# Kernel optimization log

Measured on AMD Instinct MI355X. Metric: run time of the kernel, lower is better.

The kernel has to match this reference:

```python
import jax, jax.numpy as jnp
import numpy as np

B, N, D = 8, 8192, 3
C = 64
M = 2048          # num_samples
K = 32            # max_neighbors
RADIUS = 0.3
OUT = 128
EXP = 4
CIN = C + D       # 67
HID = CIN * EXP   # 268
EPS = 1e-6        # flax LayerNorm default


def setup_inputs() -> dict:
    key = jax.random.key(0)
    ks = jax.random.split(key, 6)
    return {
        "x": jax.random.normal(ks[0], (B, N, D), jnp.float32),
        "features": jax.random.normal(ks[1], (B, N, C), jnp.float32),
        "first_idx": jax.random.randint(ks[2], (B,), 0, N, jnp.int32),
        "w1": jax.random.normal(ks[3], (CIN, HID), jnp.float32) / np.float32(np.sqrt(CIN)),
        "b1": jnp.zeros((HID,), jnp.float32),
        "g1": jnp.ones((HID,), jnp.float32),
        "be1": jnp.zeros((HID,), jnp.float32),
        "w2": jax.random.normal(ks[4], (HID, OUT), jnp.float32) / np.float32(np.sqrt(HID)),
        "b2": jnp.zeros((OUT,), jnp.float32),
        "g2": jnp.ones((OUT,), jnp.float32),
        "be2": jnp.zeros((OUT,), jnp.float32),
    }


def _layernorm(h, g, b):
    mu = jnp.mean(h, axis=-1, keepdims=True)
    var = jnp.mean(jnp.square(h), axis=-1, keepdims=True) - jnp.square(mu)
    return (h - mu) * jax.lax.rsqrt(var + EPS) * g + b


def _fps(x, first_idx, num_samples):
    # Sequential farthest-point sampling via lax.scan.
    batch = jnp.arange(x.shape[0])
    sel = jnp.full((x.shape[0], num_samples), -1, dtype=jnp.int32)
    sel = sel.at[:, 0].set(first_idx)
    first_pts = x[batch, first_idx]                       # (B,3)
    dists = jnp.sum((x - first_pts[:, None, :]) ** 2, -1)  # (B,N)

    def step(carry, i):
        s, d = carry
        far = jnp.argmax(d, axis=-1)
        s = s.at[:, i].set(far.astype(jnp.int32))
        fp = x[batch, far]
        d = jnp.minimum(d, jnp.sum((x - fp[:, None, :]) ** 2, -1))
        return (s, d), None

    (sel, _), _ = jax.lax.scan(step, (sel, dists), jnp.arange(1, num_samples))
    return sel


def _ball_query(centers, points, radius, max_neighbors):
    # centers (B,M,3), points (B,N,3) -> (B,M,K) indices, -1 where invalid
    d2 = jnp.sum((centers[:, :, None, :] - points[:, None, :, :]) ** 2, -1)  # (B,M,N)
    within = d2 < radius ** 2
    nbr = jnp.argsort(jnp.where(within, d2, 1e10), axis=-1)[:, :, :max_neighbors]
    nd = jnp.take_along_axis(d2, nbr, axis=-1)
    return jnp.where(nd < radius ** 2, nbr, -1)


def reference(x, features, first_idx, w1, b1, g1, be1, w2, b2, g2, be2):
    batch = jnp.arange(B)[:, None]                 # (B,1)
    sel = _fps(x, first_idx, M)                    # (B,M)
    centers = x[batch, sel]                        # (B,M,3)
    nbr = _ball_query(centers, x, RADIUS, K)       # (B,M,K); -1 wraps to last point (as original)
    bI = batch[:, :, None]                         # (B,1,1)
    nf = features[bI, nbr]                         # (B,M,K,C)
    npts = x[bI, nbr]                              # (B,M,K,3)
    rel = npts - centers[:, :, None, :]
    comb = jnp.concatenate([nf, rel], axis=-1)     # (B,M,K,C+3)
    h = jax.nn.gelu(comb @ w1 + b1)                # (B,M,K,HID), tanh-approx gelu as flax default
    h = _layernorm(h, g1, be1)
    h = h @ w2 + b2                                # (B,M,K,OUT)
    h = _layernorm(h, g2, be2)
    out = jnp.max(h, axis=2)                       # (B,M,OUT)
    return (centers, out)
```

## Files before the change

kernel.cpp:

```cpp
#include <hip/hip_runtime.h>
#include <hip/hip_bf16.h>
#include <math.h>

#define B_ 8
#define N_ 8192
#define C_ 64
#define M_ 2048
#define K_ 32
#define OUT_ 128
#define CIN_ 67
#define HID_ 268
#define EPS_ 1e-6f
#define CONS_ 240
#define CAPQ_ 512

typedef short short8 __attribute__((ext_vector_type(8)));
typedef float floatx4 __attribute__((ext_vector_type(4)));

__device__ __forceinline__ unsigned short f2bf(float f) {
  unsigned u = __builtin_bit_cast(unsigned, f);
  u += 0x7fffu + ((u >> 16) & 1u);
  return (unsigned short)(u >> 16);
}
__device__ __forceinline__ float bf2f(unsigned short h) {
  return __builtin_bit_cast(float, (unsigned)h << 16);
}

__device__ __forceinline__ float d2fma(float ax, float ay, float az,
                                       float bx, float by, float bz) {
#pragma clang fp contract(off)
  float dx = ax - bx, dy = ay - by, dz = az - bz;
  return __builtin_fmaf(dz, dz, __builtin_fmaf(dy, dy, dx * dx));
}

__device__ __forceinline__ float gelu_tanh(float v) {
  const float k0 = 0.7978845608028654f;
  const float k1 = 0.044715f;
  float u = k0 * (v + k1 * v * v * v);
  return 0.5f * v * (1.0f + tanhf(u));
}

__device__ __forceinline__ int msp4(int v) {
  return (v & 1) | ((v & 2) << 2) | ((v & 4) << 4) | ((v & 8) << 6);
}

template <int CTRL>
__device__ __forceinline__ unsigned long long dpp_umax64(unsigned long long k) {
  int lo = (int)(unsigned)k;
  int hi = (int)(unsigned)(k >> 32);
  unsigned slo = (unsigned)__builtin_amdgcn_update_dpp(0, lo, CTRL, 0xF, 0xF, true);
  unsigned shi = (unsigned)__builtin_amdgcn_update_dpp(0, hi, CTRL, 0xF, 0xF, true);
  unsigned long long o = ((unsigned long long)shi << 32) | (unsigned long long)slo;
  return k > o ? k : o;
}

__global__ __launch_bounds__(256) void pack_kernel(
    const float* __restrict__ w1, const float* __restrict__ w2,
    unsigned short* __restrict__ w1p, unsigned short* __restrict__ w2p,
    int* __restrict__ prog) {
  if (blockIdx.x == 0) prog[threadIdx.x] = 0;
  int e = blockIdx.x * 256 + threadIdx.x;
  if (e < 3 * 17 * 64 * 8) {
    int j = e & 7, lane = (e >> 3) & 63, fi = e >> 9;
    int kt = fi / 17, nt = fi - kt * 17;
    int k = kt * 32 + (lane >> 4) * 8 + j;
    int n = nt * 16 + (lane & 15);
    float v = (k < CIN_ && n < HID_) ? w1[k * HID_ + n] : 0.f;
    w1p[e] = f2bf(v);
  } else {
    int e2 = e - 3 * 17 * 64 * 8;
    if (e2 < 9 * 8 * 64 * 8) {
      int j = e2 & 7, lane = (e2 >> 3) & 63, fi = e2 >> 9;
      int kt = fi >> 3, nt = fi & 7;
      int k = kt * 32 + (lane >> 4) * 8 + j;
      int n = nt * 16 + (lane & 15);
      float v = (k < HID_) ? w2[k * OUT_ + n] : 0.f;
      w2p[e2] = f2bf(v);
    }
  }
}

__global__ __launch_bounds__(512) void fused_kernel(
    const float* __restrict__ x, const float* __restrict__ features,
    const int* __restrict__ first_idx,
    const unsigned short* __restrict__ w1p, const float* __restrict__ b1,
    const float* __restrict__ g1, const float* __restrict__ be1,
    const unsigned short* __restrict__ w2p, const float* __restrict__ b2,
    const float* __restrict__ g2, const float* __restrict__ be2,
    float* __restrict__ centers, float* __restrict__ out1,
    int* __restrict__ prog) {
  __shared__ __align__(16) char smem[131456];
  const int tid = threadIdx.x;
  const int lane = tid & 63;
  const int wv = tid >> 6;

  if (blockIdx.x < B_) {
    const int b = blockIdx.x;
    const float* xb = x + (size_t)b * N_ * 3;

    float* s_xyz = (float*)smem;
    char* s_mem = smem + 98304;
    unsigned long long* s_wkey = (unsigned long long*)(smem + 131072);
    int* s_wsum = (int*)(smem + 131200);
    float* s_bb = (float*)(smem + 131232);

    int* s_hist = (int*)s_mem;
    unsigned short* s_perm = (unsigned short*)(s_mem + 16384);
    float* s_cbuf = (float*)s_mem;

    {
      const float4* src = (const float4*)xb;
      float4* dst = (float4*)s_xyz;
#pragma unroll
      for (int i = 0; i < 12; ++i) {
        int e = tid + i * 512;
        dst[e] = src[e];
      }
    }
    for (int i = tid; i < 4096; i += 512) s_hist[i] = 0;
    __syncthreads();

    float bx0 = INFINITY, bx1 = -INFINITY, by0 = INFINITY, by1 = -INFINITY,
          bz0 = INFINITY, bz1 = -INFINITY;
#pragma unroll
    for (int i = 0; i < 16; ++i) {
      int p = tid + i * 512;
      float X = s_xyz[p * 3 + 0], Y = s_xyz[p * 3 + 1], Z = s_xyz[p * 3 + 2];
      bx0 = fminf(bx0, X); bx1 = fmaxf(bx1, X);
      by0 = fminf(by0, Y); by1 = fmaxf(by1, Y);
      bz0 = fminf(bz0, Z); bz1 = fmaxf(bz1, Z);
    }
#pragma unroll
    for (int off = 1; off < 64; off <<= 1) {
      bx0 = fminf(bx0, __shfl_xor(bx0, off)); bx1 = fmaxf(bx1, __shfl_xor(bx1, off));
      by0 = fminf(by0, __shfl_xor(by0, off)); by1 = fmaxf(by1, __shfl_xor(by1, off));
      bz0 = fminf(bz0, __shfl_xor(bz0, off)); bz1 = fmaxf(bz1, __shfl_xor(bz1, off));
    }
    if (lane == 0) {
      s_bb[wv * 6 + 0] = bx0; s_bb[wv * 6 + 1] = bx1; s_bb[wv * 6 + 2] = by0;
      s_bb[wv * 6 + 3] = by1; s_bb[wv * 6 + 4] = bz0; s_bb[wv * 6 + 5] = bz1;
    }
    __syncthreads();
#pragma unroll
    for (int w = 0; w < 8; ++w) {
      bx0 = fminf(bx0, s_bb[w * 6 + 0]); bx1 = fmaxf(bx1, s_bb[w * 6 + 1]);
      by0 = fminf(by0, s_bb[w * 6 + 2]); by1 = fmaxf(by1, s_bb[w * 6 + 3]);
      bz0 = fminf(bz0, s_bb[w * 6 + 4]); bz1 = fmaxf(bz1, s_bb[w * 6 + 5]);
    }
    const float kS = 16.0f * (1.0f - 1e-6f);
    float rx = bx1 - bx0, ry = by1 - by0, rz = bz1 - bz0;
    float sxv = rx > 0.f ? kS / rx : 0.f;
    float syv = ry > 0.f ? kS / ry : 0.f;
    float szv = rz > 0.f ? kS / rz : 0.f;

#pragma unroll
    for (int i = 0; i < 16; ++i) {
      int p = tid + i * 512;
      int qx = (int)((s_xyz[p * 3 + 0] - bx0) * sxv);
      int qy = (int)((s_xyz[p * 3 + 1] - by0) * syv);
      int qz = (int)((s_xyz[p * 3 + 2] - bz0) * szv);
      qx = qx < 0 ? 0 : (qx > 15 ? 15 : qx);
      qy = qy < 0 ? 0 : (qy > 15 ? 15 : qy);
      qz = qz < 0 ? 0 : (qz > 15 ? 15 : qz);
      int c = msp4(qx) | (msp4(qy) << 1) | (msp4(qz) << 2);
      atomicAdd(&s_hist[c], 1);
    }
    __syncthreads();

    {
      int h[8], pre[8];
      int acc = 0;
#pragma unroll
      for (int i = 0; i < 8; ++i) { h[i] = s_hist[tid * 8 + i]; pre[i] = acc; acc += h[i]; }
      int incl = acc;
#pragma unroll
      for (int off = 1; off < 64; off <<= 1) {
        int v = __shfl_up(incl, off);
        if (lane >= off) incl += v;
      }
      int texcl = incl - acc;
      if (lane == 63) s_wsum[wv] = incl;
      __syncthreads();
      int woff = 0;
#pragma unroll
      for (int w = 0; w < 8; ++w) woff += (w < wv) ? s_wsum[w] : 0;
#pragma unroll
      for (int i = 0; i < 8; ++i) s_hist[tid * 8 + i] = woff + texcl + pre[i];
    }
    __syncthreads();

#pragma unroll
    for (int i = 0; i < 16; ++i) {
      int p = tid + i * 512;
      int qx = (int)((s_xyz[p * 3 + 0] - bx0) * sxv);
      int qy = (int)((s_xyz[p * 3 + 1] - by0) * syv);
      int qz = (int)((s_xyz[p * 3 + 2] - bz0) * szv);
      qx = qx < 0 ? 0 : (qx > 15 ? 15 : qx);
      qy = qy < 0 ? 0 : (qy > 15 ? 15 : qy);
      qz = qz < 0 ? 0 : (qz > 15 ? 15 : qz);
      int c = msp4(qx) | (msp4(qy) << 1) | (msp4(qz) << 2);
      int pos = atomicAdd(&s_hist[c], 1);
      s_perm[pos] = (unsigned short)p;
    }
    __syncthreads();

    float px[16], py[16], pz[16], d[16];
    unsigned lo32[16];
    float gx0[2], gx1[2], gy0[2], gy1[2], gz0[2], gz1[2];
#pragma unroll
    for (int g = 0; g < 2; ++g) {
      gx0[g] = INFINITY; gx1[g] = -INFINITY; gy0[g] = INFINITY;
      gy1[g] = -INFINITY; gz0[g] = INFINITY; gz1[g] = -INFINITY;
    }
#pragma unroll
    for (int i = 0; i < 16; ++i) {
      int p = (int)s_perm[tid * 16 + i];
      int g = i >> 3;
      px[i] = s_xyz[p * 3 + 0];
      py[i] = s_xyz[p * 3 + 1];
      pz[i] = s_xyz[p * 3 + 2];
      d[i] = INFINITY;
      lo32[i] = 0xFFFFFFFFu - (unsigned)p;
      gx0[g] = fminf(gx0[g], px[i]); gx1[g] = fmaxf(gx1[g], px[i]);
      gy0[g] = fminf(gy0[g], py[i]); gy1[g] = fmaxf(gy1[g], py[i]);
      gz0[g] = fminf(gz0[g], pz[i]); gz1[g] = fmaxf(gz1[g], pz[i]);
    }
    float wx0 = fminf(gx0[0], gx0[1]), wx1 = fmaxf(gx1[0], gx1[1]);
    float wy0 = fminf(gy0[0], gy0[1]), wy1 = fmaxf(gy1[0], gy1[1]);
    float wz0 = fminf(gz0[0], gz0[1]), wz1 = fmaxf(gz1[0], gz1[1]);
#pragma unroll
    for (int off = 1; off < 64; off <<= 1) {
      wx0 = fminf(wx0, __shfl_xor(wx0, off)); wx1 = fmaxf(wx1, __shfl_xor(wx1, off));
      wy0 = fminf(wy0, __shfl_xor(wy0, off)); wy1 = fmaxf(wy1, __shfl_xor(wy1, off));
      wz0 = fminf(wz0, __shfl_xor(wz0, off)); wz1 = fmaxf(wz1, __shfl_xor(wz1, off));
    }

    int fi = first_idx[b];
    float ncx = s_xyz[fi * 3 + 0], ncy = s_xyz[fi * 3 + 1], ncz = s_xyz[fi * 3 + 2];
    if (tid == 0) {
      s_cbuf[0] = ncx; s_cbuf[1] = ncy; s_cbuf[2] = ncz;
    }

    unsigned long long gkey[2];
    gkey[0] = 0x7F800000ULL << 32;
    gkey[1] = 0x7F800000ULL << 32;
    unsigned long long wk = 0x7F800000ULL << 32;

    for (int it = 1; it < M_; ++it) {
      float wdx = fmaxf(fmaxf(wx0 - ncx, ncx - wx1), 0.f);
      float wdy = fmaxf(fmaxf(wy0 - ncy, ncy - wy1), 0.f);
      float wdz = fmaxf(fmaxf(wz0 - ncz, ncz - wz1), 0.f);
      float wlb = __builtin_fmaf(wdz, wdz, __builtin_fmaf(wdy, wdy, wdx * wdx));
      float wgm = __builtin_bit_cast(float, (unsigned)(wk >> 32));
      if (__any(wlb * 0.999f < wgm)) {
#pragma unroll
        for (int g = 0; g < 2; ++g) {
          float gdx = fmaxf(fmaxf(gx0[g] - ncx, ncx - gx1[g]), 0.f);
          float gdy = fmaxf(fmaxf(gy0[g] - ncy, ncy - gy1[g]), 0.f);
          float gdz = fmaxf(fmaxf(gz0[g] - ncz, ncz - gz1[g]), 0.f);
          float glb = __builtin_fmaf(gdz, gdz, __builtin_fmaf(gdy, gdy, gdx * gdx));
          float ggm = __builtin_bit_cast(float, (unsigned)(gkey[g] >> 32));
          if (glb * 0.999f < ggm) {
            unsigned long long k[8];
#pragma unroll
            for (int i = 0; i < 8; ++i) {
              int s = g * 8 + i;
              float dd = d2fma(px[s], py[s], pz[s], ncx, ncy, ncz);
              float dm = fminf(d[s], dd);
              d[s] = dm;
              k[i] = ((unsigned long long)__builtin_bit_cast(unsigned, dm) << 32) |
                     (unsigned long long)lo32[s];
            }
#pragma unroll
            for (int sd = 4; sd >= 1; sd >>= 1)
#pragma unroll
              for (int i = 0; i < sd; ++i)
                k[i] = k[i] > k[i + sd] ? k[i] : k[i + sd];
            gkey[g] = k[0];
          }
        }
        unsigned long long kk = gkey[0] > gkey[1] ? gkey[0] : gkey[1];
        kk = dpp_umax64<0x111>(kk);
        kk = dpp_umax64<0x112>(kk);
        kk = dpp_umax64<0x114>(kk);
        kk = dpp_umax64<0x118>(kk);
        kk = dpp_umax64<0x142>(kk);
        kk = dpp_umax64<0x143>(kk);
        wk = kk;
      }
      if (lane == 63) s_wkey[(it & 1) * 8 + wv] = wk;
      __syncthreads();
      if ((it & 31) == 0) {
        if (wv == 0 && lane < 24) {
          const float4* src = (const float4*)(s_cbuf + (size_t)(it - 32) * 3);
          float4* dst = (float4*)(centers + (size_t)b * M_ * 3 + (size_t)(it - 32) * 3);
          dst[lane] = src[lane];
        }
        if (tid == 0)
          __hip_atomic_store(&prog[b * 32], it, __ATOMIC_RELEASE, __HIP_MEMORY_SCOPE_AGENT);
      }
      {
        const ulonglong2* sp = (const ulonglong2*)(&s_wkey[(it & 1) * 8]);
        ulonglong2 q0 = sp[0], q1 = sp[1], q2 = sp[2], q3 = sp[3];
        unsigned long long a0 = q0.x > q0.y ? q0.x : q0.y;
        unsigned long long a1 = q1.x > q1.y ? q1.x : q1.y;
        unsigned long long a2 = q2.x > q2.y ? q2.x : q2.y;
        unsigned long long a3 = q3.x > q3.y ? q3.x : q3.y;
        unsigned long long b0 = a0 > a1 ? a0 : a1;
        unsigned long long b1v = a2 > a3 ? a2 : a3;
        unsigned long long gk = b0 > b1v ? b0 : b1v;
        int gi = (int)(0xFFFFFFFFu - (unsigned)(gk & 0xFFFFFFFFull));
        int gs = __builtin_amdgcn_readfirstlane(gi);
        ncx = s_xyz[gs * 3 + 0];
        ncy = s_xyz[gs * 3 + 1];
        ncz = s_xyz[gs * 3 + 2];
      }
      if (tid == 0) {
        s_cbuf[it * 3 + 0] = ncx; s_cbuf[it * 3 + 1] = ncy; s_cbuf[it * 3 + 2] = ncz;
      }
    }

    __syncthreads();
    if (wv == 0 && lane < 24) {
      const float4* src = (const float4*)(s_cbuf + (size_t)(M_ - 32) * 3);
      float4* dst = (float4*)(centers + (size_t)b * M_ * 3 + (size_t)(M_ - 32) * 3);
      dst[lane] = src[lane];
    }
    if (tid == 0)
      __hip_atomic_store(&prog[b * 32], M_, __ATOMIC_RELEASE, __HIP_MEMORY_SCOPE_AGENT);

  } else {
    unsigned short* A1 = (unsigned short*)smem;
    unsigned short* H1 = (unsigned short*)(smem + 13312);
    float* H2 = (float*)(smem + 51200);
    float* cd = (float*)(smem + 84992);
    int* cidx = (int*)(smem + 89088);
    float* s_sum = (float*)(smem + 93184);
    float* s_sum2 = (float*)(smem + 93440);
    float* s_mu = (float*)(smem + 93696);
    float* s_rs = (float*)(smem + 93952);
    int* s_nbr = (int*)(smem + 94208);
    float* s_ctr = (float*)(smem + 94464);
    int* s_wc = (int*)(smem + 94496);

    const int j = (int)blockIdx.x - B_;
    const int b = j & 7;
    const int c = j >> 3;
    const int q4 = lane >> 4;
    const int nl = lane & 15;

    for (int e = tid; e < 64 * 104; e += 512) A1[e] = 0;
    for (int e = tid; e < 64 * 296; e += 512) H1[e] = 0;
    __syncthreads();

    const float* xb = x + (size_t)b * N_ * 3;

    for (int k35 = 0; k35 < 35; ++k35) {
      int i = c + 30 * k35;
      if (i >= 1024) break;
      const int m0 = 2 * i, m1 = m0 + 1;
      const int cm0 = b * M_ + m0;

      if (tid == 0) {
        if (__hip_atomic_load(&prog[b * 32], __ATOMIC_ACQUIRE,
                              __HIP_MEMORY_SCOPE_AGENT) <= m1) {
          do {
            __builtin_amdgcn_s_sleep(16);
          } while (__hip_atomic_load(&prog[b * 32], __ATOMIC_ACQUIRE,
                                     __HIP_MEMORY_SCOPE_AGENT) <= m1);
        }
      }
      __syncthreads();

      if (tid < 64) s_sum[tid] = 0.f;
      else if (tid < 128) s_sum2[tid - 64] = 0.f;
      else if (tid < 134) s_ctr[tid - 128] = centers[(size_t)cm0 * 3 + (tid - 128)];
      __syncthreads();

      const float c0x = s_ctr[0], c0y = s_ctr[1], c0z = s_ctr[2];
      const float c1x = s_ctr[3], c1y = s_ctr[4], c1z = s_ctr[5];

      int cnt0 = 0, cnt1 = 0;
      for (int s = 0; s < 16; ++s) {
        int p = wv * 1024 + s * 64 + lane;
        float X = xb[p * 3 + 0], Y = xb[p * 3 + 1], Z = xb[p * 3 + 2];
        float d20 = d2fma(X, Y, Z, c0x, c0y, c0z);
        float d21 = d2fma(X, Y, Z, c1x, c1y, c1z);
        cnt0 += (int)__popcll(__ballot(d20 < 0.09f));
        cnt1 += (int)__popcll(__ballot(d21 < 0.09f));
      }
      if (lane == 0) { s_wc[wv] = cnt0; s_wc[8 + wv] = cnt1; }
      __syncthreads();
      int base0 = 0, tot0 = 0, base1 = 0, tot1 = 0;
#pragma unroll
      for (int w = 0; w < 8; ++w) {
        int v0 = s_wc[w], v1 = s_wc[8 + w];
        base0 += (w < wv) ? v0 : 0; tot0 += v0;
        base1 += (w < wv) ? v1 : 0; tot1 += v1;
      }
      int count0 = tot0 < CAPQ_ ? tot0 : CAPQ_;
      int count1 = tot1 < CAPQ_ ? tot1 : CAPQ_;
      int pos0 = base0, pos1 = base1;
      for (int s = 0; s < 16; ++s) {
        int p = wv * 1024 + s * 64 + lane;
        float X = xb[p * 3 + 0], Y = xb[p * 3 + 1], Z = xb[p * 3 + 2];
        float d20 = d2fma(X, Y, Z, c0x, c0y, c0z);
        float d21 = d2fma(X, Y, Z, c1x, c1y, c1z);
        bool in0 = d20 < 0.09f;
        bool in1 = d21 < 0.09f;
        unsigned long long m0m = __ballot(in0);
        unsigned long long m1m = __ballot(in1);
        if (in0) {
          int pp = pos0 + (int)__popcll(m0m & ((1ull << lane) - 1ull));
          if (pp < CAPQ_) { cd[pp] = d20; cidx[pp] = p; }
        }
        if (in1) {
          int pp = pos1 + (int)__popcll(m1m & ((1ull << lane) - 1ull));
          if (pp < CAPQ_) { cd[CAPQ_ + pp] = d21; cidx[CAPQ_ + pp] = p; }
        }
        pos0 += (int)__popcll(m0m);
        pos1 += (int)__popcll(m1m);
      }
      __syncthreads();
      {
        int q = tid >> 8;
        int lt = tid & 255;
        int cnt = q ? count1 : count0;
        int nw = cnt < K_ ? cnt : K_;
        const float* cdq = cd + q * CAPQ_;
        const int* cxq = cidx + q * CAPQ_;
        for (int cc = lt; cc < cnt; cc += 256) {
          float dcc = cdq[cc];
          int rank = 0;
          for (int jj = 0; jj < cnt; ++jj) {
            float dj = cdq[jj];
            rank += (dj < dcc || (dj == dcc && jj < cc)) ? 1 : 0;
          }
          if (rank < K_) s_nbr[q * K_ + rank] = cxq[cc];
        }
        for (int s = nw + lt; s < K_; s += 256) s_nbr[q * K_ + s] = N_ - 1;
      }
      __syncthreads();

#pragma unroll
      for (int h = 0; h < 2; ++h) {
        int rr = (tid >> 4) + h * 32;
        int jj = tid & 15;
        int q = rr >> 5;
        int idx = s_nbr[rr];
        const float4* frow = (const float4*)(features + ((size_t)b * N_ + idx) * C_);
        float4 f4 = frow[jj];
        int base = rr * 104 + jj * 4;
        A1[base + 0] = f2bf(f4.x); A1[base + 1] = f2bf(f4.y);
        A1[base + 2] = f2bf(f4.z); A1[base + 3] = f2bf(f4.w);
        if (jj == 0) {
          const float* xp = x + ((size_t)b * N_ + idx) * 3;
          A1[rr * 104 + 64] = f2bf(xp[0] - s_ctr[q * 3 + 0]);
          A1[rr * 104 + 65] = f2bf(xp[1] - s_ctr[q * 3 + 1]);
          A1[rr * 104 + 66] = f2bf(xp[2] - s_ctr[q * 3 + 2]);
        }
      }
      __syncthreads();

      for (int nt = wv; nt < 17; nt += 8) {
        short8 bfr[3];
#pragma unroll
        for (int kt = 0; kt < 3; ++kt)
          bfr[kt] = *(const short8*)(w1p + (size_t)((kt * 17 + nt) * 64 + lane) * 8);
        int col = nt * 16 + nl;
        bool cok = col < HID_;
        float bias = cok ? b1[col] : 0.f;
#pragma unroll
        for (int mt = 0; mt < 4; ++mt) {
          floatx4 acc = {0.f, 0.f, 0.f, 0.f};
          const unsigned short* ap = A1 + (mt * 16 + nl) * 104 + q4 * 8;
#pragma unroll
          for (int kt = 0; kt < 3; ++kt) {
            short8 a = *(const short8*)(ap + kt * 32);
            acc = __builtin_amdgcn_mfma_f32_16x16x32_bf16(a, bfr[kt], acc, 0, 0, 0);
          }
#pragma unroll
          for (int r = 0; r < 4; ++r) {
            int row = mt * 16 + q4 * 4 + r;
            float g = 0.f;
            if (cok) {
              float v = acc[r] + bias;
              g = gelu_tanh(v);
              H1[row * 296 + col] = f2bf(g);
            }
            float s1 = g, s2 = g * g;
#pragma unroll
            for (int off = 1; off < 16; off <<= 1) {
              s1 += __shfl_xor(s1, off);
              s2 += __shfl_xor(s2, off);
            }
            if (nl == 0) { atomicAdd(&s_sum[row], s1); atomicAdd(&s_sum2[row], s2); }
          }
        }
      }
      __syncthreads();
      if (tid < 64) {
        float mu = s_sum[tid] * (1.f / HID_);
        float var = s_sum2[tid] * (1.f / HID_) - mu * mu;
        s_mu[tid] = mu;
        s_rs[tid] = rsqrtf(var + EPS_);
      }
      __syncthreads();
      for (int e = tid; e < 64 * HID_; e += 512) {
        int r = e / HID_, cc = e - r * HID_;
        float g = bf2f(H1[r * 296 + cc]);
        float v = (g - s_mu[r]) * s_rs[r] * g1[cc] + be1[cc];
        H1[r * 296 + cc] = f2bf(v);
      }
      if (tid < 64) { s_sum[tid] = 0.f; s_sum2[tid] = 0.f; }
      __syncthreads();

      {
        int nt = wv;
        short8 bfr2[9];
#pragma unroll
        for (int kt = 0; kt < 9; ++kt)
          bfr2[kt] = *(const short8*)(w2p + (size_t)((kt * 8 + nt) * 64 + lane) * 8);
        int col = nt * 16 + nl;
        float bias = b2[col];
#pragma unroll
        for (int mt = 0; mt < 4; ++mt) {
          floatx4 acc = {0.f, 0.f, 0.f, 0.f};
          const unsigned short* ap = H1 + (mt * 16 + nl) * 296 + q4 * 8;
#pragma unroll
          for (int kt = 0; kt < 9; ++kt) {
            short8 a = *(const short8*)(ap + kt * 32);
            acc = __builtin_amdgcn_mfma_f32_16x16x32_bf16(a, bfr2[kt], acc, 0, 0, 0);
          }
#pragma unroll
          for (int r = 0; r < 4; ++r) {
            int row = mt * 16 + q4 * 4 + r;
            float v = acc[r] + bias;
            H2[row * 132 + col] = v;
            float s1 = v, s2 = v * v;
#pragma unroll
            for (int off = 1; off < 16; off <<= 1) {
              s1 += __shfl_xor(s1, off);
              s2 += __shfl_xor(s2, off);
            }
            if (nl == 0) { atomicAdd(&s_sum[row], s1); atomicAdd(&s_sum2[row], s2); }
          }
        }
      }
      __syncthreads();
      if (tid < 64) {
        float mu = s_sum[tid] * (1.f / OUT_);
        float var = s_sum2[tid] * (1.f / OUT_) - mu * mu;
        s_mu[tid] = mu;
        s_rs[tid] = rsqrtf(var + EPS_);
      }
      __syncthreads();
      if (tid < 256) {
        int q = tid >> 7, col = tid & 127;
        float gg = g2[col], bb = be2[col];
        float mx = -3.4e38f;
#pragma unroll 4
        for (int r = 0; r < K_; ++r) {
          int row = q * K_ + r;
          float v = H2[row * 132 + col];
          float o = (v - s_mu[row]) * s_rs[row] * gg + bb;
          mx = fmaxf(mx, o);
        }
        out1[(size_t)(cm0 + q) * OUT_ + col] = mx;
      }
      __syncthreads();
    }
  }
}

extern "C" void kernel_launch(void* const* d_in, const int* in_sizes, int n_in,
                              void* d_out, int out_size, void* d_ws, size_t ws_size,
                              hipStream_t stream) {
  const float* x = (const float*)d_in[0];
  const float* features = (const float*)d_in[1];
  const int* first_idx = (const int*)d_in[2];
  const float* w1 = (const float*)d_in[3];
  const float* b1 = (const float*)d_in[4];
  const float* g1 = (const float*)d_in[5];
  const float* be1 = (const float*)d_in[6];
  const float* w2 = (const float*)d_in[7];
  const float* b2 = (const float*)d_in[8];
  const float* g2 = (const float*)d_in[9];
  const float* be2 = (const float*)d_in[10];

  float* centers = (float*)d_out;
  float* out1 = (float*)d_out + (size_t)B_ * M_ * 3;

  int* prog = (int*)d_ws;
  unsigned short* w1p = (unsigned short*)((char*)d_ws + 2097152);
  unsigned short* w2p = (unsigned short*)((char*)d_ws + 2149376);

  pack_kernel<<<dim3(246), dim3(256), 0, stream>>>(w1, w2, w1p, w2p, prog);
  fused_kernel<<<dim3(B_ + CONS_), dim3(512), 0, stream>>>(
      x, features, first_idx, w1p, b1, g1, be1, w2p, b2, g2, be2,
      centers, out1, prog);
}
```

Before: 1.943 ms.

## Run two interleaved FPS batches per producer block sharing one barrier

Each producer block now runs farthest-point sampling for two batches at once, each thread holding 32 points in registers, and one __syncthreads per iteration serves both batches. The idea is to let the independent dependency chains of two batches hide each other's latency and to halve the number of producer blocks. Other changes: the per-wave bounding-box early-out is dropped, centers are staged through a small 64-entry ring instead of a full buffer, the next center is read from global memory instead of LDS, and consumer spin-waits use relaxed loads with periodic acquire. Risks are higher register pressure and a longer per-iteration critical path, since each block now does twice the serial work.

```diff
diff --git a/kernel.cpp b/kernel.cpp
--- a/kernel.cpp
+++ b/kernel.cpp
@@ -11,6 +11,7 @@
 #define CIN_ 67
 #define HID_ 268
 #define EPS_ 1e-6f
+#define NPROD_ 4
 #define CONS_ 240
 #define CAPQ_ 512
 
@@ -52,6 +53,16 @@
   unsigned shi = (unsigned)__builtin_amdgcn_update_dpp(0, hi, CTRL, 0xF, 0xF, true);
   unsigned long long o = ((unsigned long long)shi << 32) | (unsigned long long)slo;
   return k > o ? k : o;
+}
+
+__device__ __forceinline__ unsigned long long wave_dpp_max64(unsigned long long kk) {
+  kk = dpp_umax64<0x111>(kk);
+  kk = dpp_umax64<0x112>(kk);
+  kk = dpp_umax64<0x114>(kk);
+  kk = dpp_umax64<0x118>(kk);
+  kk = dpp_umax64<0x142>(kk);
+  kk = dpp_umax64<0x143>(kk);
+  return kk;
 }
 
 __global__ __launch_bounds__(256) void pack_kernel(
@@ -89,218 +100,224 @@
     const float* __restrict__ g2, const float* __restrict__ be2,
     float* __restrict__ centers, float* __restrict__ out1,
     int* __restrict__ prog) {
-  __shared__ __align__(16) char smem[131456];
+  __shared__ __align__(16) char smem[133632];
   const int tid = threadIdx.x;
   const int lane = tid & 63;
   const int wv = tid >> 6;
 
-  if (blockIdx.x < B_) {
-    const int b = blockIdx.x;
-    const float* xb = x + (size_t)b * N_ * 3;
+  if (blockIdx.x < NPROD_) {
+    const int bp = blockIdx.x;
 
     float* s_xyz = (float*)smem;
-    char* s_mem = smem + 98304;
-    unsigned long long* s_wkey = (unsigned long long*)(smem + 131072);
-    int* s_wsum = (int*)(smem + 131200);
-    float* s_bb = (float*)(smem + 131232);
-
-    int* s_hist = (int*)s_mem;
-    unsigned short* s_perm = (unsigned short*)(s_mem + 16384);
-    float* s_cbuf = (float*)s_mem;
-
-    {
-      const float4* src = (const float4*)xb;
-      float4* dst = (float4*)s_xyz;
-#pragma unroll
-      for (int i = 0; i < 12; ++i) {
-        int e = tid + i * 512;
-        dst[e] = src[e];
-      }
+    int* s_hist = (int*)(smem + 98304);
+    unsigned short* s_perm = (unsigned short*)(smem + 114688);
+    float* s_ring0 = (float*)(smem + 131072);
+    float* s_ring1 = (float*)(smem + 131840);
+    unsigned long long* s_went = (unsigned long long*)(smem + 132608);
+    int* s_wsum = (int*)(smem + 132864);
+    float* s_bb = (float*)(smem + 132896);
+
+    float px[32], py[32], pz[32], d[32];
+    unsigned lo32[32];
+    float gx0[2][2], gx1[2][2], gy0[2][2], gy1[2][2], gz0[2][2], gz1[2][2];
+    float ncx[2], ncy[2], ncz[2];
+
+#pragma unroll
+    for (int h = 0; h < 2; ++h) {
+      const int b = 2 * bp + h;
+      const float* xb = x + (size_t)b * N_ * 3;
+
+      {
+        const float4* src = (const float4*)xb;
+        float4* dst = (float4*)s_xyz;
+#pragma unroll
+        for (int i = 0; i < 12; ++i) {
+          int e = tid + i * 512;
+          dst[e] = src[e];
+        }
+      }
+      for (int i = tid; i < 4096; i += 512) s_hist[i] = 0;
+      __syncthreads();
+
+      float bx0 = INFINITY, bx1 = -INFINITY, by0 = INFINITY, by1 = -INFINITY,
+            bz0 = INFINITY, bz1 = -INFINITY;
+#pragma unroll
+      for (int i = 0; i < 16; ++i) {
+        int p = tid + i * 512;
+        float X = s_xyz[p * 3 + 0], Y = s_xyz[p * 3 + 1], Z = s_xyz[p * 3 + 2];
+        bx0 = fminf(bx0, X); bx1 = fmaxf(bx1, X);
+        by0 = fminf(by0, Y); by1 = fmaxf(by1, Y);
+        bz0 = fminf(bz0, Z); bz1 = fmaxf(bz1, Z);
+      }
+#pragma unroll
+      for (int off = 1; off < 64; off <<= 1) {
+        bx0 = fminf(bx0, __shfl_xor(bx0, off)); bx1 = fmaxf(bx1, __shfl_xor(bx1, off));
+        by0 = fminf(by0, __shfl_xor(by0, off)); by1 = fmaxf(by1, __shfl_xor(by1, off));
+        bz0 = fminf(bz0, __shfl_xor(bz0, off)); bz1 = fmaxf(bz1, __shfl_xor(bz1, off));
+      }
+      if (lane == 0) {
+        s_bb[wv * 6 + 0] = bx0; s_bb[wv * 6 + 1] = bx1; s_bb[wv * 6 + 2] = by0;
+        s_bb[wv * 6 + 3] = by1; s_bb[wv * 6 + 4] = bz0; s_bb[wv * 6 + 5] = bz1;
+      }
+      __syncthreads();
+#pragma unroll
+      for (int w = 0; w < 8; ++w) {
+        bx0 = fminf(bx0, s_bb[w * 6 + 0]); bx1 = fmaxf(bx1, s_bb[w * 6 + 1]);
+        by0 = fminf(by0, s_bb[w * 6 + 2]); by1 = fmaxf(by1, s_bb[w * 6 + 3]);
+        bz0 = fminf(bz0, s_bb[w * 6 + 4]); bz1 = fmaxf(bz1, s_bb[w * 6 + 5]);
+      }
+      const float kS = 16.0f * (1.0f - 1e-6f);
+      float rx = bx1 - bx0, ry = by1 - by0, rz = bz1 - bz0;
+      float sxv = rx > 0.f ? kS / rx : 0.f;
+      float syv = ry > 0.f ? kS / ry : 0.f;
+      float szv = rz > 0.f ? kS / rz : 0.f;
+
+#pragma unroll
+      for (int i = 0; i < 16; ++i) {
+        int p = tid + i * 512;
+        int qx = (int)((s_xyz[p * 3 + 0] - bx0) * sxv);
+        int qy = (int)((s_xyz[p * 3 + 1] - by0) * syv);
+        int qz = (int)((s_xyz[p * 3 + 2] - bz0) * szv);
+        qx = qx < 0 ? 0 : (qx > 15 ? 15 : qx);
+        qy = qy < 0 ? 0 : (qy > 15 ? 15 : qy);
+        qz = qz < 0 ? 0 : (qz > 15 ? 15 : qz);
+        int cc = msp4(qx) | (msp4(qy) << 1) | (msp4(qz) << 2);
+        atomicAdd(&s_hist[cc], 1);
+      }
+      __syncthreads();
+
+      {
+        int hh[8], pre[8];
+        int acc = 0;
+#pragma unroll
+        for (int i = 0; i < 8; ++i) { hh[i] = s_hist[tid * 8 + i]; pre[i] = acc; acc += hh[i]; }
+        int incl = acc;
+#pragma unroll
+        for (int off = 1; off < 64; off <<= 1) {
+          int v = __shfl_up(incl, off);
+          if (lane >= off) incl += v;
+        }
+        int texcl = incl - acc;
+        if (lane == 63) s_wsum[wv] = incl;
+        __syncthreads();
+        int woff = 0;
+#pragma unroll
+        for (int w = 0; w < 8; ++w) woff += (w < wv) ? s_wsum[w] : 0;
+#pragma unroll
+        for (int i = 0; i < 8; ++i) s_hist[tid * 8 + i] = woff + texcl + pre[i];
+      }
+      __syncthreads();
+
+#pragma unroll
+      for (int i = 0; i < 16; ++i) {
+        int p = tid + i * 512;
+        int qx = (int)((s_xyz[p * 3 + 0] - bx0) * sxv);
+        int qy = (int)((s_xyz[p * 3 + 1] - by0) * syv);
+        int qz = (int)((s_xyz[p * 3 + 2] - bz0) * szv);
+        qx = qx < 0 ? 0 : (qx > 15 ? 15 : qx);
+        qy = qy < 0 ? 0 : (qy > 15 ? 15 : qy);
+        qz = qz < 0 ? 0 : (qz > 15 ? 15 : qz);
+        int cc = msp4(qx) | (msp4(qy) << 1) | (msp4(qz) << 2);
+        int pos = atomicAdd(&s_hist[cc], 1);
+        s_perm[pos] = (unsigned short)p;
+      }
+      __syncthreads();
+
+#pragma unroll
+      for (int g = 0; g < 2; ++g) {
+        gx0[h][g] = INFINITY; gx1[h][g] = -INFINITY; gy0[h][g] = INFINITY;
+        gy1[h][g] = -INFINITY; gz0[h][g] = INFINITY; gz1[h][g] = -INFINITY;
+      }
+#pragma unroll
+      for (int i = 0; i < 16; ++i) {
+        int p = (int)s_perm[tid * 16 + i];
+        int g = i >> 3;
+        int s = h * 16 + i;
+        px[s] = s_xyz[p * 3 + 0];
+        py[s] = s_xyz[p * 3 + 1];
+        pz[s] = s_xyz[p * 3 + 2];
+        d[s] = INFINITY;
+        lo32[s] = 0xFFFFFFFFu - (unsigned)p;
+        gx0[h][g] = fminf(gx0[h][g], px[s]); gx1[h][g] = fmaxf(gx1[h][g], px[s]);
+        gy0[h][g] = fminf(gy0[h][g], py[s]); gy1[h][g] = fmaxf(gy1[h][g], py[s]);
+        gz0[h][g] = fminf(gz0[h][g], pz[s]); gz1[h][g] = fmaxf(gz1[h][g], pz[s]);
+      }
+
+      int fi = first_idx[b];
+      ncx[h] = s_xyz[fi * 3 + 0]; ncy[h] = s_xyz[fi * 3 + 1]; ncz[h] = s_xyz[fi * 3 + 2];
+      if (tid == 0) {
+        float* r = (h ? s_ring1 : s_ring0);
+        r[0] = ncx[h]; r[1] = ncy[h]; r[2] = ncz[h];
+      }
+      __syncthreads();
     }
-    for (int i = tid; i < 4096; i += 512) s_hist[i] = 0;
-    __syncthreads();
-
-    float bx0 = INFINITY, bx1 = -INFINITY, by0 = INFINITY, by1 = -INFINITY,
-          bz0 = INFINITY, bz1 = -INFINITY;
-#pragma unroll
-    for (int i = 0; i < 16; ++i) {
-      int p = tid + i * 512;
-      float X = s_xyz[p * 3 + 0], Y = s_xyz[p * 3 + 1], Z = s_xyz[p * 3 + 2];
-      bx0 = fminf(bx0, X); bx1 = fmaxf(bx1, X);
-      by0 = fminf(by0, Y); by1 = fmaxf(by1, Y);
-      bz0 = fminf(bz0, Z); bz1 = fmaxf(bz1, Z);
-    }
-#pragma unroll
-    for (int off = 1; off < 64; off <<= 1) {
-      bx0 = fminf(bx0, __shfl_xor(bx0, off)); bx1 = fmaxf(bx1, __shfl_xor(bx1, off));
-      by0 = fminf(by0, __shfl_xor(by0, off)); by1 = fmaxf(by1, __shfl_xor(by1, off));
-      bz0 = fminf(bz0, __shfl_xor(bz0, off)); bz1 = fmaxf(bz1, __shfl_xor(bz1, off));
-    }
-    if (lane == 0) {
-      s_bb[wv * 6 + 0] = bx0; s_bb[wv * 6 + 1] = bx1; s_bb[wv * 6 + 2] = by0;
-      s_bb[wv * 6 + 3] = by1; s_bb[wv * 6 + 4] = bz0; s_bb[wv * 6 + 5] = bz1;
-    }
-    __syncthreads();
-#pragma unroll
-    for (int w = 0; w < 8; ++w) {
-      bx0 = fminf(bx0, s_bb[w * 6 + 0]); bx1 = fmaxf(bx1, s_bb[w * 6 + 1]);
-      by0 = fminf(by0, s_bb[w * 6 + 2]); by1 = fmaxf(by1, s_bb[w * 6 + 3]);
-      bz0 = fminf(bz0, s_bb[w * 6 + 4]); bz1 = fmaxf(bz1, s_bb[w * 6 + 5]);
-    }
-    const float kS = 16.0f * (1.0f - 1e-6f);
-    float rx = bx1 - bx0, ry = by1 - by0, rz = bz1 - bz0;
-    float sxv = rx > 0.f ? kS / rx : 0.f;
-    float syv = ry > 0.f ? kS / ry : 0.f;
-    float szv = rz > 0.f ? kS / rz : 0.f;
-
-#pragma unroll
-    for (int i = 0; i < 16; ++i) {
-      int p = tid + i * 512;
-      int qx = (int)((s_xyz[p * 3 + 0] - bx0) * sxv);
-      int qy = (int)((s_xyz[p * 3 + 1] - by0) * syv);
-      int qz = (int)((s_xyz[p * 3 + 2] - bz0) * szv);
-      qx = qx < 0 ? 0 : (qx > 15 ? 15 : qx);
-      qy = qy < 0 ? 0 : (qy > 15 ? 15 : qy);
-      qz = qz < 0 ? 0 : (qz > 15 ? 15 : qz);
-      int c = msp4(qx) | (msp4(qy) << 1) | (msp4(qz) << 2);
-      atomicAdd(&s_hist[c], 1);
-    }
-    __syncthreads();
-
-    {
-      int h[8], pre[8];
-      int acc = 0;
-#pragma unroll
-      for (int i = 0; i < 8; ++i) { h[i] = s_hist[tid * 8 + i]; pre[i] = acc; acc += h[i]; }
-      int incl = acc;
-#pragma unroll
-      for (int off = 1; off < 64; off <<= 1) {
-        int v = __shfl_up(incl, off);
-        if (lane >= off) incl += v;
-      }
-      int texcl = incl - acc;
-      if (lane == 63) s_wsum[wv] = incl;
-      __syncthreads();
-      int woff = 0;
-#pragma unroll
-      for (int w = 0; w < 8; ++w) woff += (w < wv) ? s_wsum[w] : 0;
-#pragma unroll
-      for (int i = 0; i < 8; ++i) s_hist[tid * 8 + i] = woff + texcl + pre[i];
-    }
-    __syncthreads();
-
-#pragma unroll
-    for (int i = 0; i < 16; ++i) {
-      int p = tid + i * 512;
-      int qx = (int)((s_xyz[p * 3 + 0] - bx0) * sxv);
-      int qy = (int)((s_xyz[p * 3 + 1] - by0) * syv);
-      int qz = (int)((s_xyz[p * 3 + 2] - bz0) * szv);
-      qx = qx < 0 ? 0 : (qx > 15 ? 15 : qx);
-      qy = qy < 0 ? 0 : (qy > 15 ? 15 : qy);
-      qz = qz < 0 ? 0 : (qz > 15 ? 15 : qz);
-      int c = msp4(qx) | (msp4(qy) << 1) | (msp4(qz) << 2);
-      int pos = atomicAdd(&s_hist[c], 1);
-      s_perm[pos] = (unsigned short)p;
-    }
-    __syncthreads();
-
-    float px[16], py[16], pz[16], d[16];
-    unsigned lo32[16];
-    float gx0[2], gx1[2], gy0[2], gy1[2], gz0[2], gz1[2];
-#pragma unroll
-    for (int g = 0; g < 2; ++g) {
-      gx0[g] = INFINITY; gx1[g] = -INFINITY; gy0[g] = INFINITY;
-      gy1[g] = -INFINITY; gz0[g] = INFINITY; gz1[g] = -INFINITY;
-    }
-#pragma unroll
-    for (int i = 0; i < 16; ++i) {
-      int p = (int)s_perm[tid * 16 + i];
-      int g = i >> 3;
-      px[i] = s_xyz[p * 3 + 0];
-      py[i] = s_xyz[p * 3 + 1];
-      pz[i] = s_xyz[p * 3 + 2];
-      d[i] = INFINITY;
-      lo32[i] = 0xFFFFFFFFu - (unsigned)p;
-      gx0[g] = fminf(gx0[g], px[i]); gx1[g] = fmaxf(gx1[g], px[i]);
-      gy0[g] = fminf(gy0[g], py[i]); gy1[g] = fmaxf(gy1[g], py[i]);
-      gz0[g] = fminf(gz0[g], pz[i]); gz1[g] = fmaxf(gz1[g], pz[i]);
-    }
-    float wx0 = fminf(gx0[0], gx0[1]), wx1 = fmaxf(gx1[0], gx1[1]);
-    float wy0 = fminf(gy0[0], gy0[1]), wy1 = fmaxf(gy1[0], gy1[1]);
-    float wz0 = fminf(gz0[0], gz0[1]), wz1 = fmaxf(gz1[0], gz1[1]);
-#pragma unroll
-    for (int off = 1; off < 64; off <<= 1) {
-      wx0 = fminf(wx0, __shfl_xor(wx0, off)); wx1 = fmaxf(wx1, __shfl_xor(wx1, off));
-      wy0 = fminf(wy0, __shfl_xor(wy0, off)); wy1 = fmaxf(wy1, __shfl_xor(wy1, off));
-      wz0 = fminf(wz0, __shfl_xor(wz0, off)); wz1 = fmaxf(wz1, __shfl_xor(wz1, off));
-    }
-
-    int fi = first_idx[b];
-    float ncx = s_xyz[fi * 3 + 0], ncy = s_xyz[fi * 3 + 1], ncz = s_xyz[fi * 3 + 2];
-    if (tid == 0) {
-      s_cbuf[0] = ncx; s_cbuf[1] = ncy; s_cbuf[2] = ncz;
-    }
-
-    unsigned long long gkey[2];
-    gkey[0] = 0x7F800000ULL << 32;
-    gkey[1] = 0x7F800000ULL << 32;
-    unsigned long long wk = 0x7F800000ULL << 32;
+
+    unsigned long long gkey[2][2], wk[2];
+    gkey[0][0] = 0x7F800000ULL << 32; gkey[0][1] = 0x7F800000ULL << 32;
+    gkey[1][0] = 0x7F800000ULL << 32; gkey[1][1] = 0x7F800000ULL << 32;
+    wk[0] = 0x7F800000ULL << 32; wk[1] = 0x7F800000ULL << 32;
 
     for (int it = 1; it < M_; ++it) {
-      float wdx = fmaxf(fmaxf(wx0 - ncx, ncx - wx1), 0.f);
-      float wdy = fmaxf(fmaxf(wy0 - ncy, ncy - wy1), 0.f);
-      float wdz = fmaxf(fmaxf(wz0 - ncz, ncz - wz1), 0.f);
-      float wlb = __builtin_fmaf(wdz, wdz, __builtin_fmaf(wdy, wdy, wdx * wdx));
-      float wgm = __builtin_bit_cast(float, (unsigned)(wk >> 32));
-      if (__any(wlb * 0.999f < wgm)) {
+      const int par = it & 1;
+#pragma unroll
+      for (int h = 0; h < 2; ++h) {
+        float nx = ncx[h], ny = ncy[h], nz = ncz[h];
+        bool tr[2];
 #pragma unroll
         for (int g = 0; g < 2; ++g) {
-          float gdx = fmaxf(fmaxf(gx0[g] - ncx, ncx - gx1[g]), 0.f);
-          float gdy = fmaxf(fmaxf(gy0[g] - ncy, ncy - gy1[g]), 0.f);
-          float gdz = fmaxf(fmaxf(gz0[g] - ncz, ncz - gz1[g]), 0.f);
+          float gdx = fmaxf(fmaxf(gx0[h][g] - nx, nx - gx1[h][g]), 0.f);
+          float gdy = fmaxf(fmaxf(gy0[h][g] - ny, ny - gy1[h][g]), 0.f);
+          float gdz = fmaxf(fmaxf(gz0[h][g] - nz, nz - gz1[h][g]), 0.f);
           float glb = __builtin_fmaf(gdz, gdz, __builtin_fmaf(gdy, gdy, gdx * gdx));
-          float ggm = __builtin_bit_cast(float, (unsigned)(gkey[g] >> 32));
-          if (glb * 0.999f < ggm) {
-            unsigned long long k[8];
-#pragma unroll
-            for (int i = 0; i < 8; ++i) {
-              int s = g * 8 + i;
-              float dd = d2fma(px[s], py[s], pz[s], ncx, ncy, ncz);
-              float dm = fminf(d[s], dd);
-              d[s] = dm;
-              k[i] = ((unsigned long long)__builtin_bit_cast(unsigned, dm) << 32) |
-                     (unsigned long long)lo32[s];
+          float ggm = __builtin_bit_cast(float, (unsigned)(gkey[h][g] >> 32));
+          tr[g] = glb * 0.999f < ggm;
+        }
+        if (__any(tr[0] || tr[1])) {
+#pragma unroll
+          for (int g = 0; g < 2; ++g) {
+            if (tr[g]) {
+              unsigned long long k[8];
+#pragma unroll
+              for (int i = 0; i < 8; ++i) {
+                int s = h * 16 + g * 8 + i;
+                float dd = d2fma(px[s], py[s], pz[s], nx, ny, nz);
+                float dm = fminf(d[s], dd);
+                d[s] = dm;
+                k[i] = ((unsigned long long)__builtin_bit_cast(unsigned, dm) << 32) |
+                       (unsigned long long)lo32[s];
+              }
+#pragma unroll
+              for (int sd = 4; sd >= 1; sd >>= 1)
+#pragma unroll
+                for (int i = 0; i < sd; ++i)
+                  k[i] = k[i] > k[i + sd] ? k[i] : k[i + sd];
+              gkey[h][g] = k[0];
             }
-#pragma unroll
-            for (int sd = 4; sd >= 1; sd >>= 1)
-#pragma unroll
-              for (int i = 0; i < sd; ++i)
-                k[i] = k[i] > k[i + sd] ? k[i] : k[i + sd];
-            gkey[g] = k[0];
           }
-        }
-        unsigned long long kk = gkey[0] > gkey[1] ? gkey[0] : gkey[1];
-        kk = dpp_umax64<0x111>(kk);
-        kk = dpp_umax64<0x112>(kk);
-        kk = dpp_umax64<0x114>(kk);
-        kk = dpp_umax64<0x118>(kk);
-        kk = dpp_umax64<0x142>(kk);
-        kk = dpp_umax64<0x143>(kk);
-        wk = kk;
-      }
-      if (lane == 63) s_wkey[(it & 1) * 8 + wv] = wk;
-      __syncthreads();
+          unsigned long long kk = gkey[h][0] > gkey[h][1] ? gkey[h][0] : gkey[h][1];
+          wk[h] = wave_dpp_max64(kk);
+        }
+        if (lane == 63) s_went[(par * 2 + h) * 8 + wv] = wk[h];
+      }
+      __syncthreads();
+
       if ((it & 31) == 0) {
-        if (wv == 0 && lane < 24) {
-          const float4* src = (const float4*)(s_cbuf + (size_t)(it - 32) * 3);
-          float4* dst = (float4*)(centers + (size_t)b * M_ * 3 + (size_t)(it - 32) * 3);
+        if (wv < 2 && lane < 24) {
+          const float* ring = (wv ? s_ring1 : s_ring0);
+          const float4* src = (const float4*)(ring + ((it - 32) & 63) * 3);
+          float4* dst = (float4*)(centers + (size_t)(2 * bp + wv) * M_ * 3 +
+                                  (size_t)(it - 32) * 3);
           dst[lane] = src[lane];
         }
-        if (tid == 0)
-          __hip_atomic_store(&prog[b * 32], it, __ATOMIC_RELEASE, __HIP_MEMORY_SCOPE_AGENT);
-      }
-      {
-        const ulonglong2* sp = (const ulonglong2*)(&s_wkey[(it & 1) * 8]);
+        if (lane == 0 && wv < 2)
+          __hip_atomic_store(&prog[(2 * bp + wv) * 32], it, __ATOMIC_RELEASE,
+                             __HIP_MEMORY_SCOPE_AGENT);
+      }
+
+      int gs[2];
+#pragma unroll
+      for (int h = 0; h < 2; ++h) {
+        const ulonglong2* sp = (const ulonglong2*)(&s_went[(par * 2 + h) * 8]);
         ulonglong2 q0 = sp[0], q1 = sp[1], q2 = sp[2], q3 = sp[3];
         unsigned long long a0 = q0.x > q0.y ? q0.x : q0.y;
         unsigned long long a1 = q1.x > q1.y ? q1.x : q1.y;
@@ -310,24 +327,30 @@
         unsigned long long b1v = a2 > a3 ? a2 : a3;
         unsigned long long gk = b0 > b1v ? b0 : b1v;
         int gi = (int)(0xFFFFFFFFu - (unsigned)(gk & 0xFFFFFFFFull));
-        int gs = __builtin_amdgcn_readfirstlane(gi);
-        ncx = s_xyz[gs * 3 + 0];
-        ncy = s_xyz[gs * 3 + 1];
-        ncz = s_xyz[gs * 3 + 2];
-      }
-      if (tid == 0) {
-        s_cbuf[it * 3 + 0] = ncx; s_cbuf[it * 3 + 1] = ncy; s_cbuf[it * 3 + 2] = ncz;
+        gs[h] = __builtin_amdgcn_readfirstlane(gi);
+      }
+#pragma unroll
+      for (int h = 0; h < 2; ++h) {
+        const float* xw = x + ((size_t)(2 * bp + h) * N_ + gs[h]) * 3;
+        ncx[h] = xw[0]; ncy[h] = xw[1]; ncz[h] = xw[2];
+        if (tid == 0) {
+          float* r = (h ? s_ring1 : s_ring0) + (it & 63) * 3;
+          r[0] = ncx[h]; r[1] = ncy[h]; r[2] = ncz[h];
+        }
       }
     }
 
     __syncthreads();
-    if (wv == 0 && lane < 24) {
-      const float4* src = (const float4*)(s_cbuf + (size_t)(M_ - 32) * 3);
-      float4* dst = (float4*)(centers + (size_t)b * M_ * 3 + (size_t)(M_ - 32) * 3);
+    if (wv < 2 && lane < 24) {
+      const float* ring = (wv ? s_ring1 : s_ring0);
+      const float4* src = (const float4*)(ring + ((M_ - 32) & 63) * 3);
+      float4* dst = (float4*)(centers + (size_t)(2 * bp + wv) * M_ * 3 +
+                              (size_t)(M_ - 32) * 3);
       dst[lane] = src[lane];
     }
-    if (tid == 0)
-      __hip_atomic_store(&prog[b * 32], M_, __ATOMIC_RELEASE, __HIP_MEMORY_SCOPE_AGENT);
+    if (lane == 0 && wv < 2)
+      __hip_atomic_store(&prog[(2 * bp + wv) * 32], M_, __ATOMIC_RELEASE,
+                         __HIP_MEMORY_SCOPE_AGENT);
 
   } else {
     unsigned short* A1 = (unsigned short*)smem;
@@ -343,7 +366,7 @@
     float* s_ctr = (float*)(smem + 94464);
     int* s_wc = (int*)(smem + 94496);
 
-    const int j = (int)blockIdx.x - B_;
+    const int j = (int)blockIdx.x - NPROD_;
     const int b = j & 7;
     const int c = j >> 3;
     const int q4 = lane >> 4;
@@ -362,13 +385,19 @@
       const int cm0 = b * M_ + m0;
 
       if (tid == 0) {
-        if (__hip_atomic_load(&prog[b * 32], __ATOMIC_ACQUIRE,
-                              __HIP_MEMORY_SCOPE_AGENT) <= m1) {
-          do {
-            __builtin_amdgcn_s_sleep(16);
-          } while (__hip_atomic_load(&prog[b * 32], __ATOMIC_ACQUIRE,
-                                     __HIP_MEMORY_SCOPE_AGENT) <= m1);
-        }
+        int v = __hip_atomic_load(&prog[b * 32], __ATOMIC_RELAXED,
+                                  __HIP_MEMORY_SCOPE_AGENT);
+        int spins = 0;
+        while (v <= m1) {
+          __builtin_amdgcn_s_sleep(32);
+          v = ((++spins & 7) == 0)
+                  ? __hip_atomic_load(&prog[b * 32], __ATOMIC_ACQUIRE,
+                                      __HIP_MEMORY_SCOPE_AGENT)
+                  : __hip_atomic_load(&prog[b * 32], __ATOMIC_RELAXED,
+                                      __HIP_MEMORY_SCOPE_AGENT);
+        }
+        (void)__hip_atomic_load(&prog[b * 32], __ATOMIC_ACQUIRE,
+                                __HIP_MEMORY_SCOPE_AGENT);
       }
       __syncthreads();
 
@@ -443,8 +472,8 @@
       __syncthreads();
 
 #pragma unroll
-      for (int h = 0; h < 2; ++h) {
-        int rr = (tid >> 4) + h * 32;
+      for (int hh = 0; hh < 2; ++hh) {
+        int rr = (tid >> 4) + hh * 32;
         int jj = tid & 15;
         int q = rr >> 5;
         int idx = s_nbr[rr];
@@ -596,7 +625,7 @@
   unsigned short* w2p = (unsigned short*)((char*)d_ws + 2149376);
 
   pack_kernel<<<dim3(246), dim3(256), 0, stream>>>(w1, w2, w1p, w2p, prog);
-  fused_kernel<<<dim3(B_ + CONS_), dim3(512), 0, stream>>>(
+  fused_kernel<<<dim3(NPROD_ + CONS_), dim3(512), 0, stream>>>(
       x, features, first_idx, w1p, b1, g1, be1, w2p, b2, g2, be2,
       centers, out1, prog);
 }
```

After: 3.072 ms. +58.1%, slower.
